# Kernel tuning notes

Measured on AMD Instinct MI355X. Metric: run time of the kernel, lower is better.

## Reference

```python
import jax, jax.numpy as jnp
import numpy as np

DIM_IN = 1024
DIM_OUT = 1024
NUM_HEADS = 16
HEAD_DIM = DIM_OUT // NUM_HEADS


def setup_inputs() -> dict:
    key = jax.random.key(0)
    k1, k2, k3, k4 = jax.random.split(key, 4)
    X = jax.random.normal(k1, (4, 2048, DIM_IN), dtype=jnp.float32)
    W_qkv = jax.random.normal(k2, (DIM_IN, 3 * DIM_OUT), dtype=jnp.float32) * (DIM_IN ** -0.5)
    W_out = jax.random.normal(k3, (DIM_OUT, DIM_OUT), dtype=jnp.float32) * (DIM_OUT ** -0.5)
    b_out = jax.random.normal(k4, (DIM_OUT,), dtype=jnp.float32) * 0.01
    return {"X": X, "W_qkv": W_qkv, "W_out": W_out, "b_out": b_out}


def reference(X, W_qkv, W_out, b_out):
    B, S, _ = X.shape
    qkv = X @ W_qkv  # [B, S, 3*dim_out]
    qkv = qkv.reshape(B, S, 3, NUM_HEADS, HEAD_DIM).transpose(2, 0, 3, 1, 4)
    q, k, v = qkv[0], qkv[1], qkv[2]  # each [B, H, S, hd]
    scores = jnp.einsum('bhqd,bhkd->bhqk', q, k)  # [B, H, S, S]
    causal = jnp.triu(jnp.ones((S, S), dtype=bool), k=1)
    scores = jnp.where(causal, -jnp.inf, scores)
    attn = jax.nn.softmax(scores * (HEAD_DIM ** -0.5), axis=-1)
    ctx = jnp.einsum('bhqk,bhkd->bhqd', attn, v)  # [B, H, S, hd]
    ctx = ctx.transpose(0, 2, 1, 3).reshape(B, S, DIM_OUT)
    return ctx @ W_out + b_out
```

## Files before the change

kernel.cpp:

```cpp
#include <hip/hip_runtime.h>
#include <hip/hip_bf16.h>

typedef __bf16 bf16_t;
typedef __bf16 bf16x8 __attribute__((ext_vector_type(8)));
typedef __bf16 bf16x4 __attribute__((ext_vector_type(4)));
typedef float f32x4 __attribute__((ext_vector_type(4)));

#define AS1(p) ((const __attribute__((address_space(1))) void*)(p))
#define AS3(p) ((__attribute__((address_space(3))) void*)(p))

#define QSCALE 0.1803368801111204f

__global__ void cast_x_kernel(const float* __restrict__ X, bf16_t* __restrict__ Xb) {
  int i = (blockIdx.x * 256 + threadIdx.x) * 4;
  float4 v = *(const float4*)(X + i);
  bf16x4 o;
  o[0] = (bf16_t)v.x; o[1] = (bf16_t)v.y; o[2] = (bf16_t)v.z; o[3] = (bf16_t)v.w;
  *(bf16x4*)(Xb + i) = o;
}

__global__ void transpose_cast_kernel(const float* __restrict__ W, bf16_t* __restrict__ Wt,
                                      int K, int N) {
  __shared__ float tile[32][33];
  int n0 = blockIdx.x * 32, k0 = blockIdx.y * 32;
  int tx = threadIdx.x, ty = threadIdx.y;
  for (int r = ty; r < 32; r += 8)
    tile[r][tx] = W[(size_t)(k0 + r) * N + n0 + tx];
  __syncthreads();
  for (int r = ty; r < 32; r += 8)
    Wt[(size_t)(n0 + r) * K + k0 + tx] = (bf16_t)tile[tx][r];
}

__global__ __launch_bounds__(256) void gemm_qkv_kernel(
    const bf16_t* __restrict__ A, const bf16_t* __restrict__ Bt,
    bf16_t* __restrict__ Qb, bf16_t* __restrict__ Kb, bf16_t* __restrict__ Vt) {
  __shared__ __align__(16) bf16_t As[128 * 32];
  __shared__ __align__(16) bf16_t Bs[128 * 32];
  const int tid = threadIdx.x;
  const int lane = tid & 63, wave = tid >> 6;
  const int quad = lane >> 4, l15 = lane & 15;
  const int wr = wave >> 1, wc = wave & 1;
  const int m0 = blockIdx.x * 128, n0 = blockIdx.y * 128;
  f32x4 acc[4][4];
  const f32x4 vzero = {0.f, 0.f, 0.f, 0.f};
#pragma unroll
  for (int i = 0; i < 4; i++)
#pragma unroll
    for (int j = 0; j < 4; j++) acc[i][j] = vzero;

  for (int kb = 0; kb < 1024; kb += 32) {
    __syncthreads();
#pragma unroll
    for (int i = 0; i < 2; i++) {
      int c = i * 256 + tid;
      int row = c >> 2, kc = c & 3;
      __builtin_amdgcn_global_load_lds(AS1(A + (size_t)(m0 + row) * 1024 + kb + kc * 8),
                                       AS3(As + c * 8), 16, 0, 0);
    }
#pragma unroll
    for (int i = 0; i < 2; i++) {
      int c = i * 256 + tid;
      int row = c >> 2, kc = c & 3;
      __builtin_amdgcn_global_load_lds(AS1(Bt + (size_t)(n0 + row) * 1024 + kb + kc * 8),
                                       AS3(Bs + c * 8), 16, 0, 0);
    }
    __builtin_amdgcn_s_waitcnt(0);
    __syncthreads();
    bf16x8 af[4], bfr[4];
#pragma unroll
    for (int t = 0; t < 4; t++) {
      af[t]  = *(const bf16x8*)(As + (wr * 64 + t * 16 + l15) * 32 + quad * 8);
      bfr[t] = *(const bf16x8*)(Bs + (wc * 64 + t * 16 + l15) * 32 + quad * 8);
    }
#pragma unroll
    for (int mt = 0; mt < 4; mt++)
#pragma unroll
      for (int nt = 0; nt < 4; nt++)
        acc[mt][nt] = __builtin_amdgcn_mfma_f32_16x16x32_bf16(af[mt], bfr[nt], acc[mt][nt], 0, 0, 0);
  }
#pragma unroll
  for (int nt = 0; nt < 4; nt++) {
    int gn = n0 + wc * 64 + nt * 16 + l15;
    int which = gn >> 10;
    int rem = gn & 1023;
    int hh = rem >> 6, dd = rem & 63;
    if (which == 2) {
#pragma unroll
      for (int mt = 0; mt < 4; mt++) {
        int gm0 = m0 + wr * 64 + mt * 16 + quad * 4;
        int b = gm0 >> 11, s = gm0 & 2047;
        bf16x4 o;
#pragma unroll
        for (int r = 0; r < 4; r++) o[r] = (bf16_t)acc[mt][nt][r];
        *(bf16x4*)(Vt + ((size_t)((b << 4) + hh) * 64 + dd) * 2048 + s) = o;
      }
    } else {
      bf16_t* dst = (which == 0) ? Qb : Kb;
      float scl = (which == 0) ? QSCALE : 1.0f;
#pragma unroll
      for (int mt = 0; mt < 4; mt++) {
#pragma unroll
        for (int r = 0; r < 4; r++) {
          int gm = m0 + wr * 64 + mt * 16 + quad * 4 + r;
          int b = gm >> 11, s = gm & 2047;
          dst[((size_t)((b << 4) + hh) * 2048 + s) * 64 + dd] = (bf16_t)(acc[mt][nt][r] * scl);
        }
      }
    }
  }
}

__global__ __launch_bounds__(256, 2) void attn_kernel(
    const bf16_t* __restrict__ Qg_, const bf16_t* __restrict__ Kg_,
    const bf16_t* __restrict__ Vtg_, bf16_t* __restrict__ ctx) {
  __shared__ __align__(16) bf16_t Ks[128 * 72];
  __shared__ __align__(16) bf16_t Vst[64 * 136];
  __shared__ __align__(16) bf16_t Ps[128 * 128];
  const int tid = threadIdx.x;
  const int lane = tid & 63, w = tid >> 6;
  const int quad = lane >> 4, l15 = lane & 15;

  const int bh = blockIdx.x >> 3;
  const int pp = blockIdx.x & 7;
  const int b = bh >> 4, h = bh & 15;
  const size_t base = (size_t)bh * 2048 * 64;
  const bf16_t* Kg = Kg_ + base;
  const bf16_t* Vtg = Vtg_ + base;

  bf16x8 bone;
#pragma unroll
  for (int e = 0; e < 8; e++) bone[e] = (bf16_t)1.0f;

  bf16x8 kr[4], vr[4];
#pragma unroll
  for (int i = 0; i < 4; i++) {
    int c = i * 256 + tid;
    int r = c >> 3, dc = c & 7;
    kr[i] = *(const bf16x8*)(Kg + (size_t)r * 64 + dc * 8);
  }
#pragma unroll
  for (int i = 0; i < 4; i++) {
    int c = i * 256 + tid;
    int r = c >> 4, cc = c & 15;
    vr[i] = *(const bf16x8*)(Vtg + (size_t)r * 2048 + cc * 8);
  }

  const f32x4 vzero = {0.f, 0.f, 0.f, 0.f};

  for (int ti = 0; ti < 2; ti++) {
    const int qb = (ti == 0) ? pp : 15 - pp;
    const int L = qb + 1;

    bf16x8 aq[2][2];
#pragma unroll
    for (int mt = 0; mt < 2; mt++)
#pragma unroll
      for (int ks = 0; ks < 2; ks++)
        aq[mt][ks] = *(const bf16x8*)(Qg_ + base +
                                      (size_t)(qb * 128 + w * 32 + mt * 16 + l15) * 64 +
                                      ks * 32 + quad * 8);

    f32x4 Oacc[2][4], Lacc[2];
#pragma unroll
    for (int mt = 0; mt < 2; mt++) {
#pragma unroll
      for (int dt = 0; dt < 4; dt++) Oacc[mt][dt] = vzero;
      Lacc[mt] = vzero;
    }

    for (int j = 0; j < L; j++) {
      __syncthreads();
#pragma unroll
      for (int i = 0; i < 4; i++) {
        int c = i * 256 + tid;
        int r = c >> 3, dc = c & 7;
        *(bf16x8*)(Ks + r * 72 + dc * 8) = kr[i];
      }
#pragma unroll
      for (int i = 0; i < 4; i++) {
        int c = i * 256 + tid;
        int r = c >> 4, cc = c & 15;
        *(bf16x8*)(Vst + r * 136 + cc * 8) = vr[i];
      }
      __syncthreads();

      const bool havenext = (j + 1 < L) || (ti == 0);
      if (havenext) {
        const int jn = (j + 1 < L) ? j + 1 : 0;
#pragma unroll
        for (int i = 0; i < 4; i++) {
          int c = i * 256 + tid;
          int r = c >> 3, dc = c & 7;
          kr[i] = *(const bf16x8*)(Kg + ((size_t)jn * 128 + r) * 64 + dc * 8);
        }
#pragma unroll
        for (int i = 0; i < 4; i++) {
          int c = i * 256 + tid;
          int r = c >> 4, cc = c & 15;
          vr[i] = *(const bf16x8*)(Vtg + (size_t)r * 2048 + jn * 128 + cc * 8);
        }
      }

      const bool diag = (j == L - 1);

#pragma unroll
      for (int half = 0; half < 2; half++) {
        f32x4 sch[4][2];
#pragma unroll
        for (int nt4 = 0; nt4 < 4; nt4++) {
          const int nt = half * 4 + nt4;
          bf16x8 bk0 = *(const bf16x8*)(Ks + (nt * 16 + l15) * 72 + 0 * 32 + quad * 8);
          bf16x8 bk1 = *(const bf16x8*)(Ks + (nt * 16 + l15) * 72 + 1 * 32 + quad * 8);
#pragma unroll
          for (int mt = 0; mt < 2; mt++) {
            f32x4 s = __builtin_amdgcn_mfma_f32_16x16x32_bf16(aq[mt][0], bk0, vzero, 0, 0, 0);
            sch[nt4][mt] = __builtin_amdgcn_mfma_f32_16x16x32_bf16(aq[mt][1], bk1, s, 0, 0, 0);
          }
        }
#pragma unroll
        for (int nt4 = 0; nt4 < 4; nt4++) {
          const int nt = half * 4 + nt4;
          const int cc = 2 * nt + (l15 >> 3);
          const int pc = (cc ^ (quad << 1)) * 8 + (l15 & 7);
#pragma unroll
          for (int mt = 0; mt < 2; mt++) {
            const int prow = w * 32 + mt * 16 + quad * 4;
#pragma unroll
            for (int r = 0; r < 4; r++) {
              float x = sch[nt4][mt][r];
              if (diag) {
                int kg = (L - 1) * 128 + nt * 16 + l15;
                int qg = qb * 128 + prow + r;
                if (kg > qg) x = -INFINITY;
              }
              Ps[(prow + r) * 128 + pc] = (bf16_t)__builtin_exp2f(x);
            }
          }
        }
      }

#pragma unroll
      for (int ks = 0; ks < 4; ks++) {
        const int pcc = ((ks * 4 + quad) ^ ((l15 >> 2) << 1)) * 8;
        bf16x8 ap[2];
#pragma unroll
        for (int mt = 0; mt < 2; mt++) {
          ap[mt] = *(const bf16x8*)(Ps + (w * 32 + mt * 16 + l15) * 128 + pcc);
          Lacc[mt] = __builtin_amdgcn_mfma_f32_16x16x32_bf16(ap[mt], bone, Lacc[mt], 0, 0, 0);
        }
#pragma unroll
        for (int dt = 0; dt < 4; dt++) {
          bf16x8 bv = *(const bf16x8*)(Vst + (dt * 16 + l15) * 136 + ks * 32 + quad * 8);
#pragma unroll
          for (int mt = 0; mt < 2; mt++)
            Oacc[mt][dt] = __builtin_amdgcn_mfma_f32_16x16x32_bf16(ap[mt], bv, Oacc[mt][dt], 0, 0, 0);
        }
      }
    }

#pragma unroll
    for (int mt = 0; mt < 2; mt++) {
      float rl[4];
#pragma unroll
      for (int r = 0; r < 4; r++) rl[r] = __builtin_amdgcn_rcpf(Lacc[mt][r]);
#pragma unroll
      for (int dt = 0; dt < 4; dt++)
#pragma unroll
        for (int r = 0; r < 4; r++) {
          int qg = qb * 128 + w * 32 + mt * 16 + quad * 4 + r;
          ctx[((size_t)b * 2048 + qg) * 1024 + h * 64 + dt * 16 + l15] =
              (bf16_t)(Oacc[mt][dt][r] * rl[r]);
        }
    }
  }
}

__global__ __launch_bounds__(256) void gemm_out_kernel(
    const bf16_t* __restrict__ A, const bf16_t* __restrict__ Bt,
    const float* __restrict__ bias, float* __restrict__ out) {
  __shared__ __align__(16) bf16_t As[128 * 32];
  __shared__ __align__(16) bf16_t Bs[128 * 32];
  const int tid = threadIdx.x;
  const int lane = tid & 63, wave = tid >> 6;
  const int quad = lane >> 4, l15 = lane & 15;
  const int wr = wave >> 1, wc = wave & 1;
  const int m0 = blockIdx.x * 128, n0 = blockIdx.y * 128;
  f32x4 acc[4][4];
  const f32x4 vzero = {0.f, 0.f, 0.f, 0.f};
#pragma unroll
  for (int i = 0; i < 4; i++)
#pragma unroll
    for (int j = 0; j < 4; j++) acc[i][j] = vzero;

  for (int kb = 0; kb < 1024; kb += 32) {
    __syncthreads();
#pragma unroll
    for (int i = 0; i < 2; i++) {
      int c = i * 256 + tid;
      int row = c >> 2, kc = c & 3;
      __builtin_amdgcn_global_load_lds(AS1(A + (size_t)(m0 + row) * 1024 + kb + kc * 8),
                                       AS3(As + c * 8), 16, 0, 0);
    }
#pragma unroll
    for (int i = 0; i < 2; i++) {
      int c = i * 256 + tid;
      int row = c >> 2, kc = c & 3;
      __builtin_amdgcn_global_load_lds(AS1(Bt + (size_t)(n0 + row) * 1024 + kb + kc * 8),
                                       AS3(Bs + c * 8), 16, 0, 0);
    }
    __builtin_amdgcn_s_waitcnt(0);
    __syncthreads();
    bf16x8 af[4], bfr[4];
#pragma unroll
    for (int t = 0; t < 4; t++) {
      af[t]  = *(const bf16x8*)(As + (wr * 64 + t * 16 + l15) * 32 + quad * 8);
      bfr[t] = *(const bf16x8*)(Bs + (wc * 64 + t * 16 + l15) * 32 + quad * 8);
    }
#pragma unroll
    for (int mt = 0; mt < 4; mt++)
#pragma unroll
      for (int nt = 0; nt < 4; nt++)
        acc[mt][nt] = __builtin_amdgcn_mfma_f32_16x16x32_bf16(af[mt], bfr[nt], acc[mt][nt], 0, 0, 0);
  }
#pragma unroll
  for (int nt = 0; nt < 4; nt++) {
    int gn = n0 + wc * 64 + nt * 16 + l15;
    float bv = bias[gn];
#pragma unroll
    for (int mt = 0; mt < 4; mt++) {
#pragma unroll
      for (int r = 0; r < 4; r++) {
        int gm = m0 + wr * 64 + mt * 16 + quad * 4 + r;
        out[(size_t)gm * 1024 + gn] = acc[mt][nt][r] + bv;
      }
    }
  }
}

extern "C" void kernel_launch(void* const* d_in, const int* in_sizes, int n_in,
                              void* d_out, int out_size, void* d_ws, size_t ws_size,
                              hipStream_t stream) {
  (void)in_sizes; (void)n_in; (void)out_size; (void)ws_size;
  const float* X     = (const float*)d_in[0];
  const float* W_qkv = (const float*)d_in[1];
  const float* W_out = (const float*)d_in[2];
  const float* b_out = (const float*)d_in[3];
  float* out = (float*)d_out;

  char* ws = (char*)d_ws;
  bf16_t* Xb    = (bf16_t*)(ws);
  bf16_t* Wqkvt = (bf16_t*)(ws + 16777216);
  bf16_t* Woutt = (bf16_t*)(ws + 23068672);
  bf16_t* Qb    = (bf16_t*)(ws + 25165824);
  bf16_t* Kb    = (bf16_t*)(ws + 41943040);
  bf16_t* Vt    = (bf16_t*)(ws + 58720256);
  bf16_t* ctx   = (bf16_t*)(ws + 75497472);

  cast_x_kernel<<<8192, 256, 0, stream>>>(X, Xb);
  transpose_cast_kernel<<<dim3(96, 32), dim3(32, 8), 0, stream>>>(W_qkv, Wqkvt, 1024, 3072);
  transpose_cast_kernel<<<dim3(32, 32), dim3(32, 8), 0, stream>>>(W_out, Woutt, 1024, 1024);
  gemm_qkv_kernel<<<dim3(64, 24), 256, 0, stream>>>(Xb, Wqkvt, Qb, Kb, Vt);
  attn_kernel<<<dim3(512), 256, 0, stream>>>(Qb, Kb, Vt, ctx);
  gemm_out_kernel<<<dim3(64, 8), 256, 0, stream>>>(ctx, Woutt, b_out, out);
}
```

Measured before the change: 274.3 us.

## Rewrite attention inner loop with 32x32 MFMA, register-resident P and async LDS double-buffering

```diff
diff --git a/kernel.cpp b/kernel.cpp
--- a/kernel.cpp
+++ b/kernel.cpp
@@ -5,6 +5,8 @@
 typedef __bf16 bf16x8 __attribute__((ext_vector_type(8)));
 typedef __bf16 bf16x4 __attribute__((ext_vector_type(4)));
 typedef float f32x4 __attribute__((ext_vector_type(4)));
+typedef float f32x16 __attribute__((ext_vector_type(16)));
+typedef unsigned int u32x4 __attribute__((ext_vector_type(4)));
 
 #define AS1(p) ((const __attribute__((address_space(1))) void*)(p))
 #define AS3(p) ((__attribute__((address_space(3))) void*)(p))
@@ -110,167 +112,144 @@
   }
 }
 
+__device__ inline unsigned pack_bf16x2(float a, float b) {
+  unsigned short lo = __builtin_bit_cast(unsigned short, (bf16_t)a);
+  unsigned short hi = __builtin_bit_cast(unsigned short, (bf16_t)b);
+  return (unsigned)lo | ((unsigned)hi << 16);
+}
+
 __global__ __launch_bounds__(256, 2) void attn_kernel(
     const bf16_t* __restrict__ Qg_, const bf16_t* __restrict__ Kg_,
     const bf16_t* __restrict__ Vtg_, bf16_t* __restrict__ ctx) {
-  __shared__ __align__(16) bf16_t Ks[128 * 72];
-  __shared__ __align__(16) bf16_t Vst[64 * 136];
-  __shared__ __align__(16) bf16_t Ps[128 * 128];
+  __shared__ __align__(16) bf16_t Ksm[2][128 * 64];
+  __shared__ __align__(16) bf16_t Vsm[2][64 * 128];
+  __shared__ float Lsh[128];
   const int tid = threadIdx.x;
   const int lane = tid & 63, w = tid >> 6;
-  const int quad = lane >> 4, l15 = lane & 15;
+  const int l31 = lane & 31, hl = lane >> 5;
 
   const int bh = blockIdx.x >> 3;
   const int pp = blockIdx.x & 7;
   const int b = bh >> 4, h = bh & 15;
   const size_t base = (size_t)bh * 2048 * 64;
+  const bf16_t* Qg = Qg_ + base;
   const bf16_t* Kg = Kg_ + base;
   const bf16_t* Vtg = Vtg_ + base;
 
-  bf16x8 bone;
-#pragma unroll
-  for (int e = 0; e < 8; e++) bone[e] = (bf16_t)1.0f;
-
-  bf16x8 kr[4], vr[4];
-#pragma unroll
-  for (int i = 0; i < 4; i++) {
-    int c = i * 256 + tid;
-    int r = c >> 3, dc = c & 7;
-    kr[i] = *(const bf16x8*)(Kg + (size_t)r * 64 + dc * 8);
-  }
-#pragma unroll
-  for (int i = 0; i < 4; i++) {
-    int c = i * 256 + tid;
-    int r = c >> 4, cc = c & 15;
-    vr[i] = *(const bf16x8*)(Vtg + (size_t)r * 2048 + cc * 8);
-  }
-
-  const f32x4 vzero = {0.f, 0.f, 0.f, 0.f};
+  auto stage_kv = [&](int bb, int jn) {
+#pragma unroll
+    for (int i = 0; i < 4; i++) {
+      int slot = i * 256 + tid;
+      int row = slot >> 3, c = (slot & 7) ^ (row & 7);
+      __builtin_amdgcn_global_load_lds(AS1(Kg + ((size_t)jn * 128 + row) * 64 + c * 8),
+                                       AS3(&Ksm[bb][0] + slot * 8), 16, 0, 0);
+    }
+#pragma unroll
+    for (int i = 0; i < 4; i++) {
+      int slot = i * 256 + tid;
+      int d = slot >> 4, c = (slot & 15) ^ (d & 15);
+      __builtin_amdgcn_global_load_lds(AS1(Vtg + (size_t)d * 2048 + jn * 128 + c * 8),
+                                       AS3(&Vsm[bb][0] + slot * 8), 16, 0, 0);
+    }
+  };
+
+  int cur = 0;
+  stage_kv(0, 0);
 
   for (int ti = 0; ti < 2; ti++) {
     const int qb = (ti == 0) ? pp : 15 - pp;
     const int L = qb + 1;
-
-    bf16x8 aq[2][2];
-#pragma unroll
-    for (int mt = 0; mt < 2; mt++)
-#pragma unroll
-      for (int ks = 0; ks < 2; ks++)
-        aq[mt][ks] = *(const bf16x8*)(Qg_ + base +
-                                      (size_t)(qb * 128 + w * 32 + mt * 16 + l15) * 64 +
-                                      ks * 32 + quad * 8);
-
-    f32x4 Oacc[2][4], Lacc[2];
-#pragma unroll
-    for (int mt = 0; mt < 2; mt++) {
-#pragma unroll
-      for (int dt = 0; dt < 4; dt++) Oacc[mt][dt] = vzero;
-      Lacc[mt] = vzero;
-    }
+    const int qg = qb * 128 + w * 32 + l31;
+
+    bf16x8 aq[4];
+#pragma unroll
+    for (int kk = 0; kk < 4; kk++)
+      aq[kk] = *(const bf16x8*)(Qg + (size_t)qg * 64 + kk * 16 + hl * 8);
+
+    f32x16 Oacc[2];
+#pragma unroll
+    for (int nv = 0; nv < 2; nv++)
+#pragma unroll
+      for (int e = 0; e < 16; e++) Oacc[nv][e] = 0.f;
+    float Lpart = 0.f;
 
     for (int j = 0; j < L; j++) {
+      asm volatile("s_waitcnt vmcnt(0)" ::: "memory");
       __syncthreads();
-#pragma unroll
-      for (int i = 0; i < 4; i++) {
-        int c = i * 256 + tid;
-        int r = c >> 3, dc = c & 7;
-        *(bf16x8*)(Ks + r * 72 + dc * 8) = kr[i];
+      const bool havenext = (j + 1 < L) || (ti == 0);
+      if (havenext) stage_kv(cur ^ 1, (j + 1 < L) ? j + 1 : 0);
+
+      const bf16_t* Kb = &Ksm[cur][0];
+      const bf16_t* Vb = &Vsm[cur][0];
+      const bool diag = (j == qb);
+      const int ntmax = diag ? (w + 1) : 4;
+
+      for (int nt = 0; nt < ntmax; nt++) {
+        f32x16 sc;
+#pragma unroll
+        for (int e = 0; e < 16; e++) sc[e] = 0.f;
+        __builtin_amdgcn_s_setprio(1);
+#pragma unroll
+        for (int kk = 0; kk < 4; kk++) {
+          bf16x8 ak = *(const bf16x8*)(Kb + ((nt * 32 + l31) * 8 + ((kk * 2 + hl) ^ (l31 & 7))) * 8);
+          sc = __builtin_amdgcn_mfma_f32_32x32x16_bf16(ak, aq[kk], sc, 0, 0, 0);
+        }
+        __builtin_amdgcn_s_setprio(0);
+
+        float p[16];
+        const bool me = diag && (nt == w);
+#pragma unroll
+        for (int r = 0; r < 16; r++) {
+          const int koff = (r & 3) + 8 * (r >> 2) + 4 * hl;
+          p[r] = (me && (koff > l31)) ? 0.f : __builtin_exp2f(sc[r]);
+        }
+        {
+          float a0 = p[0] + p[1], a1 = p[2] + p[3], a2 = p[4] + p[5], a3 = p[6] + p[7];
+          float a4 = p[8] + p[9], a5 = p[10] + p[11], a6 = p[12] + p[13], a7 = p[14] + p[15];
+          Lpart += ((a0 + a1) + (a2 + a3)) + ((a4 + a5) + (a6 + a7));
+        }
+
+        unsigned own0 = pack_bf16x2(p[0], p[1]),   own1 = pack_bf16x2(p[2], p[3]);
+        unsigned own2 = pack_bf16x2(p[4], p[5]),   own3 = pack_bf16x2(p[6], p[7]);
+        unsigned own4 = pack_bf16x2(p[8], p[9]),   own5 = pack_bf16x2(p[10], p[11]);
+        unsigned own6 = pack_bf16x2(p[12], p[13]), own7 = pack_bf16x2(p[14], p[15]);
+        unsigned r0 = __shfl_xor(hl ? own0 : own2, 32, 64);
+        unsigned r1 = __shfl_xor(hl ? own1 : own3, 32, 64);
+        unsigned r2 = __shfl_xor(hl ? own4 : own6, 32, 64);
+        unsigned r3 = __shfl_xor(hl ? own5 : own7, 32, 64);
+        u32x4 w0, w1;
+        w0[0] = hl ? r0 : own0;  w0[1] = hl ? r1 : own1;
+        w0[2] = hl ? own2 : r0;  w0[3] = hl ? own3 : r1;
+        w1[0] = hl ? r2 : own4;  w1[1] = hl ? r3 : own5;
+        w1[2] = hl ? own6 : r2;  w1[3] = hl ? own7 : r3;
+        bf16x8 pa0 = __builtin_bit_cast(bf16x8, w0);
+        bf16x8 pa1 = __builtin_bit_cast(bf16x8, w1);
+
+        __builtin_amdgcn_s_setprio(1);
+#pragma unroll
+        for (int nv = 0; nv < 2; nv++) {
+          const int dr = nv * 32 + l31;
+          bf16x8 bv0 = *(const bf16x8*)(Vb + (dr * 16 + ((4 * nt + hl) ^ (dr & 15))) * 8);
+          Oacc[nv] = __builtin_amdgcn_mfma_f32_32x32x16_bf16(pa0, bv0, Oacc[nv], 0, 0, 0);
+          bf16x8 bv1 = *(const bf16x8*)(Vb + (dr * 16 + ((4 * nt + 2 + hl) ^ (dr & 15))) * 8);
+          Oacc[nv] = __builtin_amdgcn_mfma_f32_32x32x16_bf16(pa1, bv1, Oacc[nv], 0, 0, 0);
+        }
+        __builtin_amdgcn_s_setprio(0);
       }
-#pragma unroll
-      for (int i = 0; i < 4; i++) {
-        int c = i * 256 + tid;
-        int r = c >> 4, cc = c & 15;
-        *(bf16x8*)(Vst + r * 136 + cc * 8) = vr[i];
-      }
-      __syncthreads();
-
-      const bool havenext = (j + 1 < L) || (ti == 0);
-      if (havenext) {
-        const int jn = (j + 1 < L) ? j + 1 : 0;
-#pragma unroll
-        for (int i = 0; i < 4; i++) {
-          int c = i * 256 + tid;
-          int r = c >> 3, dc = c & 7;
-          kr[i] = *(const bf16x8*)(Kg + ((size_t)jn * 128 + r) * 64 + dc * 8);
-        }
-#pragma unroll
-        for (int i = 0; i < 4; i++) {
-          int c = i * 256 + tid;
-          int r = c >> 4, cc = c & 15;
-          vr[i] = *(const bf16x8*)(Vtg + (size_t)r * 2048 + jn * 128 + cc * 8);
-        }
-      }
-
-      const bool diag = (j == L - 1);
-
-#pragma unroll
-      for (int half = 0; half < 2; half++) {
-        f32x4 sch[4][2];
-#pragma unroll
-        for (int nt4 = 0; nt4 < 4; nt4++) {
-          const int nt = half * 4 + nt4;
-          bf16x8 bk0 = *(const bf16x8*)(Ks + (nt * 16 + l15) * 72 + 0 * 32 + quad * 8);
-          bf16x8 bk1 = *(const bf16x8*)(Ks + (nt * 16 + l15) * 72 + 1 * 32 + quad * 8);
-#pragma unroll
-          for (int mt = 0; mt < 2; mt++) {
-            f32x4 s = __builtin_amdgcn_mfma_f32_16x16x32_bf16(aq[mt][0], bk0, vzero, 0, 0, 0);
-            sch[nt4][mt] = __builtin_amdgcn_mfma_f32_16x16x32_bf16(aq[mt][1], bk1, s, 0, 0, 0);
-          }
-        }
-#pragma unroll
-        for (int nt4 = 0; nt4 < 4; nt4++) {
-          const int nt = half * 4 + nt4;
-          const int cc = 2 * nt + (l15 >> 3);
-          const int pc = (cc ^ (quad << 1)) * 8 + (l15 & 7);
-#pragma unroll
-          for (int mt = 0; mt < 2; mt++) {
-            const int prow = w * 32 + mt * 16 + quad * 4;
-#pragma unroll
-            for (int r = 0; r < 4; r++) {
-              float x = sch[nt4][mt][r];
-              if (diag) {
-                int kg = (L - 1) * 128 + nt * 16 + l15;
-                int qg = qb * 128 + prow + r;
-                if (kg > qg) x = -INFINITY;
-              }
-              Ps[(prow + r) * 128 + pc] = (bf16_t)__builtin_exp2f(x);
-            }
-          }
-        }
-      }
-
-#pragma unroll
-      for (int ks = 0; ks < 4; ks++) {
-        const int pcc = ((ks * 4 + quad) ^ ((l15 >> 2) << 1)) * 8;
-        bf16x8 ap[2];
-#pragma unroll
-        for (int mt = 0; mt < 2; mt++) {
-          ap[mt] = *(const bf16x8*)(Ps + (w * 32 + mt * 16 + l15) * 128 + pcc);
-          Lacc[mt] = __builtin_amdgcn_mfma_f32_16x16x32_bf16(ap[mt], bone, Lacc[mt], 0, 0, 0);
-        }
-#pragma unroll
-        for (int dt = 0; dt < 4; dt++) {
-          bf16x8 bv = *(const bf16x8*)(Vst + (dt * 16 + l15) * 136 + ks * 32 + quad * 8);
-#pragma unroll
-          for (int mt = 0; mt < 2; mt++)
-            Oacc[mt][dt] = __builtin_amdgcn_mfma_f32_16x16x32_bf16(ap[mt], bv, Oacc[mt][dt], 0, 0, 0);
-        }
-      }
-    }
-
-#pragma unroll
-    for (int mt = 0; mt < 2; mt++) {
-      float rl[4];
-#pragma unroll
-      for (int r = 0; r < 4; r++) rl[r] = __builtin_amdgcn_rcpf(Lacc[mt][r]);
-#pragma unroll
-      for (int dt = 0; dt < 4; dt++)
-#pragma unroll
-        for (int r = 0; r < 4; r++) {
-          int qg = qb * 128 + w * 32 + mt * 16 + quad * 4 + r;
-          ctx[((size_t)b * 2048 + qg) * 1024 + h * 64 + dt * 16 + l15] =
-              (bf16_t)(Oacc[mt][dt][r] * rl[r]);
-        }
+      cur ^= 1;
+    }
+
+    float Lf = Lpart + __shfl_xor(Lpart, 32, 64);
+    if (hl == 0) Lsh[w * 32 + l31] = Lf;
+#pragma unroll
+    for (int r = 0; r < 16; r++) {
+      const int crow = (r & 3) + 8 * (r >> 2) + 4 * hl;
+      const float rl = __builtin_amdgcn_rcpf(Lsh[w * 32 + crow]);
+      const int qrow = qb * 128 + w * 32 + crow;
+#pragma unroll
+      for (int nv = 0; nv < 2; nv++)
+        ctx[((size_t)b * 2048 + qrow) * 1024 + h * 64 + nv * 32 + l31] =
+            (bf16_t)(Oacc[nv][r] * rl);
     }
   }
 }
```

Result: faster. 268.3 us (-2.2%).
